# Kernel tuning notes

Measured on AMD Instinct MI355X. Metric: run time of the kernel, lower is better.

The kernel has to match this reference:

```python
import jax, jax.numpy as jnp
import numpy as np

# Dims: C = 8*8*4 = 256 input channels, O = 8*8*8 = 512 output channels,
# space_rank = 4, TT ranks = (4, 16, 16).

def setup_inputs() -> dict:
    key = jax.random.key(0)
    ks = jax.random.split(key, 6)
    inp = jax.random.normal(ks[0], (32, 256, 32, 32), dtype=jnp.float32)
    # space_factor: (space_rank, 1, kH, kW)
    space_factor = jax.random.normal(ks[1], (4, 1, 3, 3), dtype=jnp.float32) * 0.3
    # factors[i]: (in_i, rank_i, rank_{i+1}, out_i)
    factor0 = jax.random.normal(ks[2], (8, 4, 16, 8), dtype=jnp.float32) * 0.1
    factor1 = jax.random.normal(ks[3], (8, 16, 16, 8), dtype=jnp.float32) * 0.08
    # last_factor: (in_last, rank_last, out_last)
    last_factor = jax.random.normal(ks[4], (4, 16, 8), dtype=jnp.float32) * 0.1
    bias = jax.random.uniform(ks[5], (512,), dtype=jnp.float32, minval=-0.02, maxval=0.02)
    return {"input": inp, "space_factor": space_factor, "factor0": factor0,
            "factor1": factor1, "last_factor": last_factor, "bias": bias}


def reference(input, space_factor, factor0, factor1, last_factor, bias):
    B, C, H, W = input.shape
    sr = space_factor.shape[0]
    # Depthwise conv: each of the C channels convolved with the same
    # `space_rank` filters (torch repeat along out-channel dim + groups=C).
    w = jnp.tile(space_factor, (C, 1, 1, 1))  # (C*sr, 1, kH, kW)
    y = jax.lax.conv_general_dilated(
        input, w, window_strides=(1, 1), padding=[(1, 1), (1, 1)],
        feature_group_count=C,
        dimension_numbers=("NCHW", "OIHW", "NCHW"))  # (B, C*sr, H', W')
    Hp, Wp = y.shape[2], y.shape[3]
    # (B, n0, n1, n2, sr, H', W') with (n0,n1,n2) = input_chanel_shape
    t = y.reshape(B, 8, 8, 4, sr, Hp, Wp)
    # Contract the tiny TT cores first (optimal order found by tn.contractors.optimal):
    # chain: (n0, n1, n2, r0, o0, o1, o2) -- only ~0.5M elements.
    chain = jnp.einsum("apqx,bqry,crz->abcpxyz", factor0, factor1, last_factor)
    # One big contraction over (n0, n1, n2, r0): effectively a GEMM
    # (B*H'*W', C*sr) x (C*sr, O).
    out = jnp.einsum("nabcphw,abcpxyz->nxyzhw", t, chain)
    out = out.reshape(B, 512, Hp, Wp)
    return out + bias[None, :, None, None]
```

## Files before the change

### kernel.cpp

```cpp
#include <hip/hip_runtime.h>

typedef unsigned short ushort_t;
typedef __attribute__((ext_vector_type(8))) short bf16x8;
typedef __attribute__((ext_vector_type(8))) unsigned short ushort8;
typedef __attribute__((ext_vector_type(4))) float f32x4;

__device__ __forceinline__ unsigned short f2bf(float f) {
  union { float f; unsigned u; } x; x.f = f;
  unsigned r = x.u + 0x7FFFu + ((x.u >> 16) & 1u);
  return (unsigned short)(r >> 16);
}

__global__ __launch_bounds__(256) void chain_kernel(const float* __restrict__ f0,
                                                    const float* __restrict__ f1,
                                                    const float* __restrict__ lf,
                                                    ushort_t* __restrict__ chainT) {
  __shared__ float gs[512];
  int o = blockIdx.x;
  int z = o & 7, y = (o >> 3) & 7, x = o >> 6;
  int tid = threadIdx.x;
  #pragma unroll
  for (int i = 0; i < 2; ++i) {
    int e = tid + i * 256;
    int c = e & 3, q = (e >> 2) & 15, b = e >> 6;
    float s = 0.f;
    #pragma unroll
    for (int r = 0; r < 16; ++r)
      s += f1[((b * 16 + q) * 16 + r) * 8 + y] * lf[(c * 16 + r) * 8 + z];
    gs[e] = s;
  }
  __syncthreads();
  #pragma unroll
  for (int j = 0; j < 4; ++j) {
    int k = tid + j * 256;
    int p = k & 3, c = (k >> 2) & 3, b = (k >> 4) & 7, a = k >> 7;
    float s = 0.f;
    #pragma unroll
    for (int q = 0; q < 16; ++q)
      s += f0[((a * 4 + p) * 16 + q) * 8 + x] * gs[(b * 16 + q) * 4 + c];
    chainT[(size_t)o * 1024 + k] = f2bf(s);
  }
}

__global__ __launch_bounds__(256) void conv_kernel(const float* __restrict__ in,
                                                   const float* __restrict__ sf,
                                                   ushort_t* __restrict__ t) {
  __shared__ float in_lds[16][404];
  __shared__ float sf_l[36];
  int bid = blockIdx.x;
  int cg = bid & 15, hg = (bid >> 4) & 3, n = bid >> 6;
  int h0 = hg * 8;
  int tid = threadIdx.x;
  if (tid < 36) sf_l[tid] = sf[tid];
  for (int e = tid; e < 320; e += 256) {
    int ch = e / 20, rr = e % 20;
    in_lds[ch][(rr >> 1) * 40 + 3 + (rr & 1) * 33] = 0.f;
  }
  const float* inb = in + ((size_t)n * 256 + cg * 16) * 1024;
  #pragma unroll
  for (int i = 0; i < 5; ++i) {
    int e = tid + i * 256;
    int ch = e / 80, rem = e % 80;
    int r = rem >> 3, w4 = rem & 7;
    int hh = h0 - 1 + r;
    float4 v = make_float4(0.f, 0.f, 0.f, 0.f);
    if (hh >= 0 && hh < 32)
      v = *(const float4*)&inb[(size_t)ch * 1024 + hh * 32 + w4 * 4];
    *(float4*)&in_lds[ch][r * 40 + 4 + w4 * 4] = v;
  }
  __syncthreads();
  float sfr[36];
  #pragma unroll
  for (int i = 0; i < 36; ++i) sfr[i] = sf_l[i];
  int w = tid & 31, sub = tid >> 5;
  size_t m0 = (size_t)n * 1024 + (size_t)h0 * 32 + w;
  unsigned pw[8][4];
  #pragma unroll
  for (int b = 0; b < 2; ++b) {
    int ch = sub * 2 + b;
    float vals[10][3];
    #pragma unroll
    for (int r = 0; r < 10; ++r)
      #pragma unroll
      for (int dw = 0; dw < 3; ++dw)
        vals[r][dw] = in_lds[ch][r * 40 + 3 + w + dw];
    #pragma unroll
    for (int j = 0; j < 8; ++j) {
      float s0 = 0.f, s1 = 0.f, s2 = 0.f, s3 = 0.f;
      #pragma unroll
      for (int dr = 0; dr < 3; ++dr)
        #pragma unroll
        for (int dw = 0; dw < 3; ++dw) {
          float tv = vals[j + dr][dw];
          s0 += tv * sfr[0 * 9 + dr * 3 + dw];
          s1 += tv * sfr[1 * 9 + dr * 3 + dw];
          s2 += tv * sfr[2 * 9 + dr * 3 + dw];
          s3 += tv * sfr[3 * 9 + dr * 3 + dw];
        }
      pw[j][b * 2 + 0] = (unsigned)f2bf(s0) | ((unsigned)f2bf(s1) << 16);
      pw[j][b * 2 + 1] = (unsigned)f2bf(s2) | ((unsigned)f2bf(s3) << 16);
    }
  }
  #pragma unroll
  for (int j = 0; j < 8; ++j) {
    uint4 pk; pk.x = pw[j][0]; pk.y = pw[j][1]; pk.z = pw[j][2]; pk.w = pw[j][3];
    *(uint4*)&t[(m0 + (size_t)j * 32) * 1024 + (size_t)(cg * 64 + sub * 8)] = pk;
  }
}

#define AS1 __attribute__((address_space(1)))
#define AS3 __attribute__((address_space(3)))
#define BARRIER  __builtin_amdgcn_s_barrier()
#define LGKMCNT0 asm volatile("s_waitcnt lgkmcnt(0)" ::: "memory")
#define VMCNT4   asm volatile("s_waitcnt vmcnt(4)" ::: "memory")
#define VMCNT0   asm volatile("s_waitcnt vmcnt(0)" ::: "memory")

__global__ __launch_bounds__(512, 2) void gemm_kernel(const ushort_t* __restrict__ tA,
                                                      const ushort_t* __restrict__ tB,
                                                      const float* __restrict__ bias,
                                                      float* __restrict__ out) {
  __shared__ __align__(16) ushort_t smem[65536];
  int tid = threadIdx.x;
  int bid = blockIdx.x;
  int wg = (bid & 7) * 32 + (bid >> 3);
  int tile_m = (wg >> 1) * 256;
  int tile_n = (wg & 1) * 256;

  int lane = tid & 63, wv = tid >> 6;
  int wm2 = wv >> 2, wn4 = wv & 3;
  int lr = lane & 15, kg = lane >> 4;
  int kph0 = ((kg * 8) ^ ((lane & 7) * 8));
  int kph1 = ((32 + kg * 8) ^ ((lane & 7) * 8));
  int arow = wm2 * 128 + lr;
  int brow = wn4 * 64 + lr;

  int srow = tid >> 3;
  int scol = ((tid & 7) ^ (srow & 7)) * 8;
  const ushort_t* sA = tA + (size_t)(tile_m + srow) * 1024 + scol;
  const ushort_t* sB = tB + (size_t)(tile_n + srow) * 1024 + scol;

#define STAGE_A(buf, koff, h)                                                                  \
  __builtin_amdgcn_global_load_lds((const AS1 void*)(sA + (size_t)((h)*128) * 1024 + (koff)),  \
      (AS3 void*)&smem[(buf)*16384 + (h)*8192 + tid*8], 16, 0, 0);                             \
  __builtin_amdgcn_global_load_lds((const AS1 void*)(sA + (size_t)((h)*128+64) * 1024 + (koff)),\
      (AS3 void*)&smem[(buf)*16384 + (h)*8192 + 4096 + tid*8], 16, 0, 0);
#define STAGE_B(buf, koff, h)                                                                  \
  __builtin_amdgcn_global_load_lds((const AS1 void*)(sB + (size_t)((h)*128) * 1024 + (koff)),  \
      (AS3 void*)&smem[32768 + (buf)*16384 + (h)*8192 + tid*8], 16, 0, 0);                     \
  __builtin_amdgcn_global_load_lds((const AS1 void*)(sB + (size_t)((h)*128+64) * 1024 + (koff)),\
      (AS3 void*)&smem[32768 + (buf)*16384 + (h)*8192 + 4096 + tid*8], 16, 0, 0);

#define READ_A(dst, mbase, buf)                                                                \
  _Pragma("unroll")                                                                            \
  for (int mf = 0; mf < 4; ++mf) {                                                             \
    dst[mf][0] = *(const bf16x8*)&smem[(buf)*16384 + (arow + (mbase) + mf*16)*64 + kph0];      \
    dst[mf][1] = *(const bf16x8*)&smem[(buf)*16384 + (arow + (mbase) + mf*16)*64 + kph1];      \
  }
#define READ_B(dst, nbase, buf)                                                                \
  _Pragma("unroll")                                                                            \
  for (int nf = 0; nf < 2; ++nf) {                                                             \
    dst[nf][0] = *(const bf16x8*)&smem[32768 + (buf)*16384 + (brow + (nbase) + nf*16)*64 + kph0];\
    dst[nf][1] = *(const bf16x8*)&smem[32768 + (buf)*16384 + (brow + (nbase) + nf*16)*64 + kph1];\
  }
#define Q_MFMA(AF, BF, MB, NB)                                                                 \
  __builtin_amdgcn_s_setprio(1);                                                              \
  _Pragma("unroll")                                                                            \
  for (int mf = 0; mf < 4; ++mf)                                                               \
    _Pragma("unroll")                                                                          \
    for (int nf = 0; nf < 2; ++nf)                                                             \
      _Pragma("unroll")                                                                        \
      for (int ks = 0; ks < 2; ++ks)                                                           \
        acc[(MB) + mf][(NB) + nf] = __builtin_amdgcn_mfma_f32_16x16x32_bf16(                   \
            AF[mf][ks], BF[nf][ks], acc[(MB) + mf][(NB) + nf], 0, 0, 0);                       \
  __builtin_amdgcn_s_setprio(0);

  f32x4 acc[8][4];
  #pragma unroll
  for (int i = 0; i < 8; ++i)
    #pragma unroll
    for (int j = 0; j < 4; ++j) acc[i][j] = (f32x4){0.f, 0.f, 0.f, 0.f};

  bf16x8 a1[4][2], a2[4][2], b1[2][2], b2[2][2];

  STAGE_A(0, 0, 0) STAGE_A(0, 0, 1) STAGE_B(0, 0, 0) STAGE_B(0, 0, 1)
  STAGE_A(1, 64, 0) STAGE_A(1, 64, 1)
  VMCNT4; BARRIER;

#define ITER(I_, FULL)                                                                         \
  {                                                                                            \
    int k1 = (2*(I_)+1)*64, k2 = (2*(I_)+2)*64, k3 = (2*(I_)+3)*64;                            \
    READ_A(a1, 0, 0) READ_B(b1, 0, 0)                                                          \
    STAGE_B(1, k1, 0)                                                                          \
    Q_MFMA(a1, b1, 0, 0) BARRIER;                                                              \
    READ_B(b2, 32, 0) READ_A(a2, 64, 0)                                                        \
    STAGE_B(1, k1, 1)                                                                          \
    Q_MFMA(a1, b2, 0, 2) LGKMCNT0; BARRIER;                                                    \
    if (FULL) { STAGE_A(0, k2, 0) }                                                            \
    Q_MFMA(a2, b2, 4, 2) BARRIER;                                                              \
    if (FULL) { STAGE_A(0, k2, 1) }                                                            \
    Q_MFMA(a2, b1, 4, 0)                                                                       \
    if (FULL) { VMCNT4; } else { VMCNT0; }                                                     \
    BARRIER;                                                                                   \
    READ_A(a1, 0, 1) READ_B(b1, 0, 1)                                                          \
    if (FULL) { STAGE_B(0, k2, 0) }                                                            \
    Q_MFMA(a1, b1, 0, 0) BARRIER;                                                              \
    READ_B(b2, 32, 1) READ_A(a2, 64, 1)                                                        \
    if (FULL) { STAGE_B(0, k2, 1) }                                                            \
    Q_MFMA(a1, b2, 0, 2) LGKMCNT0; BARRIER;                                                    \
    if (FULL) { STAGE_A(1, k3, 0) }                                                            \
    Q_MFMA(a2, b2, 4, 2) BARRIER;                                                              \
    if (FULL) { STAGE_A(1, k3, 1) }                                                            \
    Q_MFMA(a2, b1, 4, 0)                                                                       \
    if (FULL) { VMCNT4; }                                                                      \
    BARRIER;                                                                                   \
  }

  for (int I = 0; I < 7; ++I) ITER(I, 1)
  ITER(7, 0)
#undef ITER

  #pragma unroll
  for (int mf = 0; mf < 8; ++mf)
    #pragma unroll
    for (int nf = 0; nf < 4; ++nf) {
      int m = tile_m + wm2 * 128 + mf * 16 + kg * 4;
      int o = tile_n + wn4 * 64 + nf * 16 + lr;
      float bv = bias[o];
      f32x4 v = acc[mf][nf];
      v[0] += bv; v[1] += bv; v[2] += bv; v[3] += bv;
      *(f32x4*)&out[(size_t)(m >> 10) * 524288 + (size_t)o * 1024 + (size_t)(m & 1023)] = v;
    }
}

extern "C" void kernel_launch(void* const* d_in, const int* in_sizes, int n_in,
                              void* d_out, int out_size, void* d_ws, size_t ws_size,
                              hipStream_t stream) {
  (void)in_sizes; (void)n_in; (void)out_size; (void)ws_size;
  const float* in   = (const float*)d_in[0];
  const float* sf   = (const float*)d_in[1];
  const float* f0   = (const float*)d_in[2];
  const float* f1   = (const float*)d_in[3];
  const float* lf   = (const float*)d_in[4];
  const float* bias = (const float*)d_in[5];
  float* out = (float*)d_out;

  char* ws = (char*)d_ws;
  ushort_t* t      = (ushort_t*)ws;
  ushort_t* chainT = (ushort_t*)(ws + 67108864);

  hipLaunchKernelGGL(chain_kernel, dim3(512),  dim3(256), 0, stream, f0, f1, lf, chainT);
  hipLaunchKernelGGL(conv_kernel,  dim3(2048), dim3(256), 0, stream, in, sf, t);
  hipLaunchKernelGGL(gemm_kernel,  dim3(256),  dim3(512), 0, stream, t, chainT, bias, out);
}
```

Measured before the change: 71.00 us.

## Reschedule GEMM main loop to front-load LDS reads and deepen global prefetch

Restructures the double-buffered GEMM main loop so all A and B fragments for a half-iteration are read from LDS up front. The global-to-LDS stage loads are redistributed across the four MFMA quarters, and the B half-tile for the next buffer is issued one phase earlier. The vmcnt wait is raised from 4 to 6 to allow more loads in flight, and the trailing barrier is removed on the last iteration. This aims to hide memory latency better, at the cost of more live registers and a riskier ordering of LDS buffer reuse.

```diff
diff --git a/kernel.cpp b/kernel.cpp
--- a/kernel.cpp
+++ b/kernel.cpp
@@ -112,7 +112,7 @@
 #define AS3 __attribute__((address_space(3)))
 #define BARRIER  __builtin_amdgcn_s_barrier()
 #define LGKMCNT0 asm volatile("s_waitcnt lgkmcnt(0)" ::: "memory")
-#define VMCNT4   asm volatile("s_waitcnt vmcnt(4)" ::: "memory")
+#define VMCNT6   asm volatile("s_waitcnt vmcnt(6)" ::: "memory")
 #define VMCNT0   asm volatile("s_waitcnt vmcnt(0)" ::: "memory")
 
 __global__ __launch_bounds__(512, 2) void gemm_kernel(const ushort_t* __restrict__ tA,
@@ -183,36 +183,41 @@
   bf16x8 a1[4][2], a2[4][2], b1[2][2], b2[2][2];
 
   STAGE_A(0, 0, 0) STAGE_A(0, 0, 1) STAGE_B(0, 0, 0) STAGE_B(0, 0, 1)
-  STAGE_A(1, 64, 0) STAGE_A(1, 64, 1)
-  VMCNT4; BARRIER;
+  STAGE_A(1, 64, 0) STAGE_A(1, 64, 1) STAGE_B(1, 64, 0)
+  VMCNT6; BARRIER;
 
 #define ITER(I_, FULL)                                                                         \
   {                                                                                            \
     int k1 = (2*(I_)+1)*64, k2 = (2*(I_)+2)*64, k3 = (2*(I_)+3)*64;                            \
-    READ_A(a1, 0, 0) READ_B(b1, 0, 0)                                                          \
-    STAGE_B(1, k1, 0)                                                                          \
-    Q_MFMA(a1, b1, 0, 0) BARRIER;                                                              \
-    READ_B(b2, 32, 0) READ_A(a2, 64, 0)                                                        \
+                                                           \
+    READ_A(a1, 0, 0) READ_A(a2, 64, 0) READ_B(b1, 0, 0) READ_B(b2, 32, 0)                      \
     STAGE_B(1, k1, 1)                                                                          \
-    Q_MFMA(a1, b2, 0, 2) LGKMCNT0; BARRIER;                                                    \
+    Q_MFMA(a1, b1, 0, 0) LGKMCNT0; BARRIER;                                                    \
+                                                                                       \
     if (FULL) { STAGE_A(0, k2, 0) }                                                            \
+    Q_MFMA(a1, b2, 0, 2) BARRIER;                                                              \
+                                                                                       \
+    if (FULL) { STAGE_A(0, k2, 1) }                                                            \
     Q_MFMA(a2, b2, 4, 2) BARRIER;                                                              \
-    if (FULL) { STAGE_A(0, k2, 1) }                                                            \
+                             \
+    if (FULL) { STAGE_B(0, k2, 0) }                                                            \
     Q_MFMA(a2, b1, 4, 0)                                                                       \
-    if (FULL) { VMCNT4; } else { VMCNT0; }                                                     \
+    if (FULL) { VMCNT6; } else { VMCNT0; }                                                     \
     BARRIER;                                                                                   \
-    READ_A(a1, 0, 1) READ_B(b1, 0, 1)                                                          \
-    if (FULL) { STAGE_B(0, k2, 0) }                                                            \
-    Q_MFMA(a1, b1, 0, 0) BARRIER;                                                              \
-    READ_B(b2, 32, 1) READ_A(a2, 64, 1)                                                        \
+                                                                       \
+    READ_A(a1, 0, 1) READ_A(a2, 64, 1) READ_B(b1, 0, 1) READ_B(b2, 32, 1)                      \
     if (FULL) { STAGE_B(0, k2, 1) }                                                            \
-    Q_MFMA(a1, b2, 0, 2) LGKMCNT0; BARRIER;                                                    \
+    Q_MFMA(a1, b1, 0, 0) LGKMCNT0; BARRIER;                                                    \
+                                                                                       \
     if (FULL) { STAGE_A(1, k3, 0) }                                                            \
+    Q_MFMA(a1, b2, 0, 2) BARRIER;                                                              \
+                                                                                       \
+    if (FULL) { STAGE_A(1, k3, 1) }                                                            \
     Q_MFMA(a2, b2, 4, 2) BARRIER;                                                              \
-    if (FULL) { STAGE_A(1, k3, 1) }                                                            \
+                                    \
+    if (FULL) { STAGE_B(1, k3, 0) }                                                            \
     Q_MFMA(a2, b1, 4, 0)                                                                       \
-    if (FULL) { VMCNT4; }                                                                      \
-    BARRIER;                                                                                   \
+    if (FULL) { VMCNT6; BARRIER; }                                                             \
   }
 
   for (int I = 0; I < 7; ++I) ITER(I, 1)
```

Result: no change. 71.07 us (+0.1%).
